# Kernel tuning notes

Hardware: AMD Instinct MI355X
Metric: run time of the kernel (lower is better)

Reference implementation:

```python
import jax, jax.numpy as jnp
import numpy as np

N_NODES = 100000
N_EDGES = 600000
D = 128          # node/edge latent dim == hs[-1]
H = 256          # hs[0] == hs[1]
LN_EPS = 1e-5


def setup_inputs() -> dict:
    key = jax.random.key(0)
    ks = jax.random.split(key, 8)
    x = jax.random.normal(ks[0], (N_NODES, D), dtype=jnp.float32)
    edge_index = jax.random.randint(ks[1], (2, N_EDGES), 0, N_NODES, dtype=jnp.int64)
    edge_attr = jax.random.normal(ks[2], (N_EDGES, D), dtype=jnp.float32)
    # MLP: Linear(256->256), SiLU, Linear(256->128); then LayerNorm(128)
    s1 = 1.0 / np.sqrt(H)
    s2 = 1.0 / np.sqrt(H)
    W1 = jax.random.uniform(ks[3], (H, H), jnp.float32, -s1, s1)
    b1 = jax.random.uniform(ks[4], (H,), jnp.float32, -s1, s1)
    W2 = jax.random.uniform(ks[5], (H, D), jnp.float32, -s2, s2)
    b2 = jax.random.uniform(ks[6], (D,), jnp.float32, -s2, s2)
    ln_gamma = jnp.ones((D,), jnp.float32)
    ln_beta = jnp.zeros((D,), jnp.float32)
    return {"x": x, "edge_index": edge_index, "edge_attr": edge_attr,
            "W1": W1, "b1": b1, "W2": W2, "b2": b2,
            "ln_gamma": ln_gamma, "ln_beta": ln_beta}


def reference(x, edge_index, edge_attr, W1, b1, W2, b2, ln_gamma, ln_beta):
    i = edge_index[0]  # destination node index (scatter target)
    # scatter-sum of edge features onto nodes: [N, D]
    agg = jax.ops.segment_sum(edge_attr, i, num_segments=x.shape[0])
    h = jnp.concatenate([x, agg], axis=-1)            # [N, 2D] == [N, H]
    h = jax.nn.silu(h @ W1 + b1)                      # Linear + SiLU
    h = h @ W2 + b2                                   # Linear (no act on last)
    # LayerNorm over last dim
    mu = jnp.mean(h, axis=-1, keepdims=True)
    var = jnp.mean(jnp.square(h - mu), axis=-1, keepdims=True)
    h = (h - mu) * jax.lax.rsqrt(var + LN_EPS) * ln_gamma + ln_beta
    return h + x                                      # residual
```

## Files before the change

kernel.cpp:

```cpp
#include <hip/hip_runtime.h>
#include <hip/hip_bf16.h>

typedef __bf16 bf16;
typedef __bf16 bf16x8 __attribute__((ext_vector_type(8)));
typedef __bf16 bf16x4v __attribute__((ext_vector_type(4)));
typedef float f32x4 __attribute__((ext_vector_type(4)));

#define NN 100000
#define NE 600000
#define SCB 2048
#define NBLK ((NN + SCB - 1) / SCB)

static __device__ __forceinline__ float silu_f(float v) {
    return v / (1.f + __expf(-v));
}

__global__ void k_probe(const void* __restrict__ gamma,
                        const void* __restrict__ eidx,
                        int* __restrict__ flags) {
    unsigned g0 = ((const unsigned*)gamma)[0];
    flags[0] = (g0 == 0x3F803F80u) ? 1 : 0;
    const int* e32 = (const int*)eidx;
    int is64 = 1;
    for (int k = 1; k < 64; k += 2)
        if (e32[k] != 0) is64 = 0;
    flags[1] = is64;
}

static __device__ __forceinline__ float load_f(const void* p, long i, int isbf) {
    return isbf ? (float)((const bf16*)p)[i] : ((const float*)p)[i];
}

static __device__ __forceinline__ bf16x8 load_row8(const void* p, long off, int isbf) {
    if (isbf) return *(const bf16x8*)((const bf16*)p + off);
    const float* f = (const float*)p + off;
    f32x4 f0 = *(const f32x4*)f;
    f32x4 f1 = *(const f32x4*)(f + 4);
    bf16x8 r;
#pragma unroll
    for (int t = 0; t < 4; t++) { r[t] = (bf16)f0[t]; r[t + 4] = (bf16)f1[t]; }
    return r;
}

__global__ __launch_bounds__(256) void k_transpose(const void* __restrict__ W1,
                                                   const void* __restrict__ W2,
                                                   bf16* __restrict__ w1t,
                                                   bf16* __restrict__ w2t,
                                                   const int* __restrict__ flags) {
    int isbf = flags[0];
    int tid = blockIdx.x * 256 + threadIdx.x;
    if (tid < 256 * 256) {
        int k = tid >> 8, n = tid & 255;
        w1t[n * 256 + k] = (bf16)load_f(W1, tid, isbf);
    } else if (tid < 256 * 256 + 256 * 128) {
        int t = tid - 256 * 256;
        int k = t >> 7, n = t & 127;
        w2t[n * 256 + k] = (bf16)load_f(W2, t, isbf);
    }
}

__global__ __launch_bounds__(256) void k_hist(const void* __restrict__ eidx,
                                              int* __restrict__ cnt,
                                              const int* __restrict__ flags) {
    int e = blockIdx.x * 256 + threadIdx.x;
    if (e >= NE) return;
    int dst = flags[1] ? (int)((const long long*)eidx)[e]
                       : ((const int*)eidx)[e];
    atomicAdd(&cnt[dst], 1);
}

__global__ __launch_bounds__(256) void k_scan1(const int* __restrict__ cnt,
                                               int* __restrict__ blksum) {
    __shared__ int red[256];
    int b = blockIdx.x, t = threadIdx.x;
    int base = b * SCB + t * 8;
    int s = 0;
#pragma unroll
    for (int i = 0; i < 8; i++) {
        int idx = base + i;
        if (idx < NN) s += cnt[idx];
    }
    red[t] = s;
    __syncthreads();
    for (int d = 128; d > 0; d >>= 1) {
        if (t < d) red[t] += red[t + d];
        __syncthreads();
    }
    if (t == 0) blksum[b] = red[0];
}

__global__ __launch_bounds__(64) void k_scan2(const int* __restrict__ blksum,
                                              int* __restrict__ blkoff) {
    int t = threadIdx.x;
    int v = (t < NBLK) ? blksum[t] : 0;
    int s = v;
#pragma unroll
    for (int d = 1; d < 64; d <<= 1) {
        int o = __shfl_up(s, d, 64);
        if (t >= d) s += o;
    }
    if (t < NBLK) blkoff[t] = s - v;
}

__global__ __launch_bounds__(256) void k_scan3(const int* __restrict__ cnt,
                                               const int* __restrict__ blkoff,
                                               int* __restrict__ off,
                                               int* __restrict__ pos) {
    __shared__ int part[256];
    int b = blockIdx.x, t = threadIdx.x;
    int base = b * SCB + t * 8;
    int v[8];
    int s = 0;
#pragma unroll
    for (int i = 0; i < 8; i++) {
        int idx = base + i;
        v[i] = (idx < NN) ? cnt[idx] : 0;
        s += v[i];
    }
    part[t] = s;
    __syncthreads();
    for (int d = 1; d < 256; d <<= 1) {
        int o = (t >= d) ? part[t - d] : 0;
        __syncthreads();
        part[t] += o;
        __syncthreads();
    }
    int run = blkoff[b] + part[t] - s;
#pragma unroll
    for (int i = 0; i < 8; i++) {
        int idx = base + i;
        if (idx < NN) { off[idx] = run; pos[idx] = run; }
        run += v[i];
    }
    if (b == 0 && t == 0) off[NN] = NE;
}

__global__ __launch_bounds__(256) void k_order(const void* __restrict__ eidx,
                                               int* __restrict__ pos,
                                               int* __restrict__ order,
                                               const int* __restrict__ flags) {
    int e = blockIdx.x * 256 + threadIdx.x;
    if (e >= NE) return;
    int dst = flags[1] ? (int)((const long long*)eidx)[e]
                       : ((const int*)eidx)[e];
    int p = atomicAdd(&pos[dst], 1);
    order[p] = e;
}

__global__ __launch_bounds__(256) void k_agg(const void* __restrict__ eattr,
                                             const int* __restrict__ order,
                                             const int* __restrict__ off,
                                             bf16* __restrict__ agg,
                                             const int* __restrict__ flags) {
    int isbf = flags[0];
    int gid = blockIdx.x * 256 + threadIdx.x;
    int node = gid >> 5;
    if (node >= NN) return;
    int c = (gid & 31) << 2;
    int beg = off[node], end = off[node + 1];
    float a0 = 0.f, a1 = 0.f, a2 = 0.f, a3 = 0.f;
    for (int e = beg; e < end; e++) {
        long id = order[e];
        if (isbf) {
            bf16x4v v = *(const bf16x4v*)((const bf16*)eattr + id * 128 + c);
            a0 += (float)v[0]; a1 += (float)v[1];
            a2 += (float)v[2]; a3 += (float)v[3];
        } else {
            f32x4 v = *(const f32x4*)((const float*)eattr + id * 128 + c);
            a0 += v[0]; a1 += v[1]; a2 += v[2]; a3 += v[3];
        }
    }
    bf16x4v r;
    r[0] = (bf16)a0; r[1] = (bf16)a1; r[2] = (bf16)a2; r[3] = (bf16)a3;
    *(bf16x4v*)(agg + (long)node * 128 + c) = r;
}

__global__ __launch_bounds__(256) void k_mlp(const void* __restrict__ x,
                                             const bf16* __restrict__ agg,
                                             const bf16* __restrict__ w1t,
                                             const void* __restrict__ b1,
                                             const bf16* __restrict__ w2t,
                                             const void* __restrict__ b2,
                                             const void* __restrict__ gamma,
                                             const void* __restrict__ beta,
                                             void* __restrict__ out,
                                             const int* __restrict__ flags) {
    __shared__ bf16 h1s[128 * 256];
    const int isbf = flags[0];
    const int tid = threadIdx.x;
    const int wave = tid >> 6, lane = tid & 63;
    const int l15 = lane & 15, quad = lane >> 4;
    const int kq = quad * 8;
    const long row0 = (long)blockIdx.x * 128;
    const int wrow = wave * 32;

    int arow[2];
#pragma unroll
    for (int i = 0; i < 2; i++) {
        long r = row0 + wrow + i * 16 + l15;
        arow[i] = (r < NN) ? (int)r : (NN - 1);
    }

    bf16x8 ax[2][4], ag[2][4];
#pragma unroll
    for (int i = 0; i < 2; i++) {
#pragma unroll
        for (int kc = 0; kc < 4; kc++) {
            ax[i][kc] = load_row8(x, (long)arow[i] * 128 + kc * 32 + kq, isbf);
            ag[i][kc] = *(const bf16x8*)(agg + (long)arow[i] * 128 + kc * 32 + kq);
        }
    }

#pragma unroll
    for (int jc = 0; jc < 4; jc++) {
        f32x4 acc[2][4] = {};
#pragma unroll
        for (int kc = 0; kc < 4; kc++) {
            bf16x8 b[4];
#pragma unroll
            for (int j = 0; j < 4; j++)
                b[j] = *(const bf16x8*)(w1t + (long)(jc * 64 + j * 16 + l15) * 256 + kc * 32 + kq);
#pragma unroll
            for (int i = 0; i < 2; i++)
#pragma unroll
                for (int j = 0; j < 4; j++)
                    acc[i][j] = __builtin_amdgcn_mfma_f32_16x16x32_bf16(ax[i][kc], b[j], acc[i][j], 0, 0, 0);
        }
#pragma unroll
        for (int kc = 0; kc < 4; kc++) {
            bf16x8 b[4];
#pragma unroll
            for (int j = 0; j < 4; j++)
                b[j] = *(const bf16x8*)(w1t + (long)(jc * 64 + j * 16 + l15) * 256 + 128 + kc * 32 + kq);
#pragma unroll
            for (int i = 0; i < 2; i++)
#pragma unroll
                for (int j = 0; j < 4; j++)
                    acc[i][j] = __builtin_amdgcn_mfma_f32_16x16x32_bf16(ag[i][kc], b[j], acc[i][j], 0, 0, 0);
        }
        float bias[4];
#pragma unroll
        for (int j = 0; j < 4; j++) bias[j] = load_f(b1, jc * 64 + j * 16 + l15, isbf);
#pragma unroll
        for (int i = 0; i < 2; i++) {
#pragma unroll
            for (int r = 0; r < 4; r++) {
                int lr = wrow + i * 16 + quad * 4 + r;
#pragma unroll
                for (int j = 0; j < 4; j++) {
                    int c = jc * 64 + j * 16 + l15;
                    int g = c >> 3, o = c & 7;
                    h1s[lr * 256 + ((g ^ (lr & 31)) << 3) + o] =
                        (bf16)silu_f(acc[i][j][r] + bias[j]);
                }
            }
        }
    }
    __syncthreads();

    f32x4 acc2[2][8] = {};
#pragma unroll
    for (int kc = 0; kc < 8; kc++) {
        bf16x8 a[2], b[8];
#pragma unroll
        for (int i = 0; i < 2; i++) {
            int lr = wrow + i * 16 + l15;
            int g = kc * 4 + quad;
            a[i] = *(const bf16x8*)(h1s + lr * 256 + ((g ^ (lr & 31)) << 3));
        }
#pragma unroll
        for (int j = 0; j < 8; j++)
            b[j] = *(const bf16x8*)(w2t + (long)(j * 16 + l15) * 256 + kc * 32 + kq);
#pragma unroll
        for (int i = 0; i < 2; i++)
#pragma unroll
            for (int j = 0; j < 8; j++)
                acc2[i][j] = __builtin_amdgcn_mfma_f32_16x16x32_bf16(a[i], b[j], acc2[i][j], 0, 0, 0);
    }

    float b2c[8], gm[8], bt[8];
#pragma unroll
    for (int j = 0; j < 8; j++) {
        int c = j * 16 + l15;
        b2c[j] = load_f(b2, c, isbf);
        gm[j] = load_f(gamma, c, isbf);
        bt[j] = load_f(beta, c, isbf);
    }

#pragma unroll
    for (int i = 0; i < 2; i++) {
#pragma unroll
        for (int r = 0; r < 4; r++) {
            long row = row0 + wrow + i * 16 + quad * 4 + r;
            float v[8], s = 0.f, s2 = 0.f;
#pragma unroll
            for (int j = 0; j < 8; j++) {
                v[j] = acc2[i][j][r] + b2c[j];
                s += v[j];
                s2 += v[j] * v[j];
            }
#pragma unroll
            for (int m = 1; m < 16; m <<= 1) {
                s += __shfl_xor(s, m, 64);
                s2 += __shfl_xor(s2, m, 64);
            }
            float mu = s * (1.f / 128.f);
            float var = s2 * (1.f / 128.f) - mu * mu;
            float rstd = rsqrtf(var + 1e-5f);
            if (row < NN) {
#pragma unroll
                for (int j = 0; j < 8; j++) {
                    int c = j * 16 + l15;
                    float o = (v[j] - mu) * rstd * gm[j] + bt[j] + load_f(x, row * 128 + c, isbf);
                    if (isbf) ((bf16*)out)[row * 128 + c] = (bf16)o;
                    else      ((float*)out)[row * 128 + c] = o;
                }
            }
        }
    }
}

extern "C" void kernel_launch(void* const* d_in, const int* in_sizes, int n_in,
                              void* d_out, int out_size, void* d_ws, size_t ws_size,
                              hipStream_t stream) {
    const void* x     = d_in[0];
    const void* eidx  = d_in[1];
    const void* eattr = d_in[2];
    const void* W1    = d_in[3];
    const void* b1    = d_in[4];
    const void* W2    = d_in[5];
    const void* b2    = d_in[6];
    const void* gamma = d_in[7];
    const void* beta  = d_in[8];

    char* ws = (char*)d_ws;
    bf16*  w1t    = (bf16*)ws;
    bf16*  w2t    = (bf16*)(ws + 131072);
    int*   flags  = (int*)(ws + 196608);
    int*   blksum = (int*)(ws + 197120);
    int*   blkoff = (int*)(ws + 197632);
    int*   cnt    = (int*)(ws + 262144);
    int*   off    = (int*)(ws + 720896);
    int*   pos    = (int*)(ws + 1179648);
    int*   order  = (int*)(ws + 1638400);
    bf16*  agg    = (bf16*)(ws + 4194304);

    k_probe<<<1, 1, 0, stream>>>(gamma, eidx, flags);
    hipMemsetAsync(cnt, 0, (size_t)NN * 4, stream);
    k_transpose<<<384, 256, 0, stream>>>(W1, W2, w1t, w2t, flags);
    k_hist<<<(NE + 255) / 256, 256, 0, stream>>>(eidx, cnt, flags);
    k_scan1<<<NBLK, 256, 0, stream>>>(cnt, blksum);
    k_scan2<<<1, 64, 0, stream>>>(blksum, blkoff);
    k_scan3<<<NBLK, 256, 0, stream>>>(cnt, blkoff, off, pos);
    k_order<<<(NE + 255) / 256, 256, 0, stream>>>(eidx, pos, order, flags);
    k_agg<<<(NN * 32) / 256, 256, 0, stream>>>(eattr, order, off, agg, flags);
    k_mlp<<<782, 256, 0, stream>>>(x, agg, w1t, b1, w2t, b2, gamma, beta, d_out, flags);
}
```

Before: 726.2 us.

## Make MLP kernel persistent with register-resident weights and LDS-staged input tiles

Rewrites the fused MLP kernel as a persistent grid of 512-thread blocks that loop over 128-row tiles. Each wave loads its slice of W1 and W2 fragments into registers once. Each tile's x and agg rows are staged cooperatively into swizzled LDS, and the output columns are split across the 8 waves, so the per-row LayerNorm sums are combined through a small LDS array. The goal is to stop re-reading weight fragments from global memory for every tile and to coalesce the input loads. In exchange it uses about 137KB of LDS per block, which likely allows only one block per CU, and adds several block-wide barriers per tile.

After: 726.9 us. About the same (+0.1%).

```diff
diff --git a/kernel.cpp b/kernel.cpp
--- a/kernel.cpp
+++ b/kernel.cpp
@@ -10,6 +10,7 @@
 #define NE 600000
 #define SCB 2048
 #define NBLK ((NN + SCB - 1) / SCB)
+#define NTILE ((NN + 127) / 128)
 
 static __device__ __forceinline__ float silu_f(float v) {
     return v / (1.f + __expf(-v));
@@ -29,17 +30,6 @@
 
 static __device__ __forceinline__ float load_f(const void* p, long i, int isbf) {
     return isbf ? (float)((const bf16*)p)[i] : ((const float*)p)[i];
-}
-
-static __device__ __forceinline__ bf16x8 load_row8(const void* p, long off, int isbf) {
-    if (isbf) return *(const bf16x8*)((const bf16*)p + off);
-    const float* f = (const float*)p + off;
-    f32x4 f0 = *(const f32x4*)f;
-    f32x4 f1 = *(const f32x4*)(f + 4);
-    bf16x8 r;
-#pragma unroll
-    for (int t = 0; t < 4; t++) { r[t] = (bf16)f0[t]; r[t + 4] = (bf16)f1[t]; }
-    return r;
 }
 
 __global__ __launch_bounds__(256) void k_transpose(const void* __restrict__ W1,
@@ -175,148 +165,166 @@
     *(bf16x4v*)(agg + (long)node * 128 + c) = r;
 }
 
-__global__ __launch_bounds__(256) void k_mlp(const void* __restrict__ x,
-                                             const bf16* __restrict__ agg,
-                                             const bf16* __restrict__ w1t,
-                                             const void* __restrict__ b1,
-                                             const bf16* __restrict__ w2t,
-                                             const void* __restrict__ b2,
-                                             const void* __restrict__ gamma,
-                                             const void* __restrict__ beta,
-                                             void* __restrict__ out,
-                                             const int* __restrict__ flags) {
+__global__ __launch_bounds__(512, 2) void k_mlp(const void* __restrict__ x,
+                                                const bf16* __restrict__ agg,
+                                                const bf16* __restrict__ w1t,
+                                                const void* __restrict__ b1,
+                                                const bf16* __restrict__ w2t,
+                                                const void* __restrict__ b2,
+                                                const void* __restrict__ gamma,
+                                                const void* __restrict__ beta,
+                                                void* __restrict__ out,
+                                                const int* __restrict__ flags) {
+    __shared__ bf16 As[128 * 256];
     __shared__ bf16 h1s[128 * 256];
+    __shared__ float2 lnred[128 * 9];
+
     const int isbf = flags[0];
     const int tid = threadIdx.x;
     const int wave = tid >> 6, lane = tid & 63;
     const int l15 = lane & 15, quad = lane >> 4;
     const int kq = quad * 8;
-    const long row0 = (long)blockIdx.x * 128;
-    const int wrow = wave * 32;
-
-    int arow[2];
-#pragma unroll
-    for (int i = 0; i < 2; i++) {
-        long r = row0 + wrow + i * 16 + l15;
-        arow[i] = (r < NN) ? (int)r : (NN - 1);
-    }
-
-    bf16x8 ax[2][4], ag[2][4];
-#pragma unroll
-    for (int i = 0; i < 2; i++) {
-#pragma unroll
-        for (int kc = 0; kc < 4; kc++) {
-            ax[i][kc] = load_row8(x, (long)arow[i] * 128 + kc * 32 + kq, isbf);
-            ag[i][kc] = *(const bf16x8*)(agg + (long)arow[i] * 128 + kc * 32 + kq);
-        }
-    }
-
-#pragma unroll
-    for (int jc = 0; jc < 4; jc++) {
-        f32x4 acc[2][4] = {};
-#pragma unroll
-        for (int kc = 0; kc < 4; kc++) {
-            bf16x8 b[4];
-#pragma unroll
-            for (int j = 0; j < 4; j++)
-                b[j] = *(const bf16x8*)(w1t + (long)(jc * 64 + j * 16 + l15) * 256 + kc * 32 + kq);
-#pragma unroll
-            for (int i = 0; i < 2; i++)
-#pragma unroll
-                for (int j = 0; j < 4; j++)
-                    acc[i][j] = __builtin_amdgcn_mfma_f32_16x16x32_bf16(ax[i][kc], b[j], acc[i][j], 0, 0, 0);
-        }
-#pragma unroll
-        for (int kc = 0; kc < 4; kc++) {
-            bf16x8 b[4];
-#pragma unroll
-            for (int j = 0; j < 4; j++)
-                b[j] = *(const bf16x8*)(w1t + (long)(jc * 64 + j * 16 + l15) * 256 + 128 + kc * 32 + kq);
-#pragma unroll
-            for (int i = 0; i < 2; i++)
-#pragma unroll
-                for (int j = 0; j < 4; j++)
-                    acc[i][j] = __builtin_amdgcn_mfma_f32_16x16x32_bf16(ag[i][kc], b[j], acc[i][j], 0, 0, 0);
-        }
-        float bias[4];
-#pragma unroll
-        for (int j = 0; j < 4; j++) bias[j] = load_f(b1, jc * 64 + j * 16 + l15, isbf);
-#pragma unroll
-        for (int i = 0; i < 2; i++) {
+
+    bf16x8 b1f[8][2], b2f[8];
+#pragma unroll
+    for (int kc = 0; kc < 8; kc++) {
+#pragma unroll
+        for (int j = 0; j < 2; j++)
+            b1f[kc][j] = *(const bf16x8*)(w1t + (long)(wave * 32 + j * 16 + l15) * 256 + kc * 32 + kq);
+        b2f[kc] = *(const bf16x8*)(w2t + (long)(wave * 16 + l15) * 256 + kc * 32 + kq);
+    }
+    float bias1[2];
+    bias1[0] = load_f(b1, wave * 32 + l15, isbf);
+    bias1[1] = load_f(b1, wave * 32 + 16 + l15, isbf);
+    const int ocol = wave * 16 + l15;
+    const float b2c = load_f(b2, ocol, isbf);
+    const float gm = load_f(gamma, ocol, isbf);
+    const float bt = load_f(beta, ocol, isbf);
+
+    for (int tile = blockIdx.x; tile < NTILE; tile += gridDim.x) {
+        const long row0 = (long)tile * 128;
+
+        if (isbf) {
+#pragma unroll
+            for (int it = 0; it < 4; it++) {
+                int idx = it * 512 + tid;
+                int r = idx >> 4, co = idx & 15;
+                long gr = row0 + r; if (gr >= NN) gr = NN - 1;
+                bf16x8 v = *(const bf16x8*)((const bf16*)x + gr * 128 + co * 8);
+                *(bf16x8*)(As + r * 256 + ((co ^ (r & 31)) << 3)) = v;
+            }
+        } else {
+#pragma unroll
+            for (int it = 0; it < 8; it++) {
+                int idx = it * 512 + tid;
+                int r = idx >> 5, cq = idx & 31;
+                long gr = row0 + r; if (gr >= NN) gr = NN - 1;
+                f32x4 v = *(const f32x4*)((const float*)x + gr * 128 + cq * 4);
+                bf16x4v h;
+#pragma unroll
+                for (int t = 0; t < 4; t++) h[t] = (bf16)v[t];
+                *(bf16x4v*)(As + r * 256 + (((cq >> 1) ^ (r & 31)) << 3) + ((cq & 1) << 2)) = h;
+            }
+        }
+#pragma unroll
+        for (int it = 0; it < 4; it++) {
+            int idx = it * 512 + tid;
+            int r = idx >> 4, co = idx & 15;
+            long gr = row0 + r; if (gr >= NN) gr = NN - 1;
+            bf16x8 v = *(const bf16x8*)(agg + gr * 128 + co * 8);
+            *(bf16x8*)(As + r * 256 + (((16 + co) ^ (r & 31)) << 3)) = v;
+        }
+        __syncthreads();
+
+#pragma unroll
+        for (int ih = 0; ih < 2; ih++) {
+            f32x4 acc[4][2] = {};
+#pragma unroll
+            for (int kc = 0; kc < 8; kc++) {
+#pragma unroll
+                for (int i2 = 0; i2 < 4; i2++) {
+                    int r = (ih * 4 + i2) * 16 + l15;
+                    bf16x8 a = *(const bf16x8*)(As + r * 256 + (((kc * 4 + quad) ^ (r & 31)) << 3));
+#pragma unroll
+                    for (int j = 0; j < 2; j++)
+                        acc[i2][j] = __builtin_amdgcn_mfma_f32_16x16x32_bf16(a, b1f[kc][j], acc[i2][j], 0, 0, 0);
+                }
+            }
+#pragma unroll
+            for (int i2 = 0; i2 < 4; i2++) {
+#pragma unroll
+                for (int j = 0; j < 2; j++) {
+#pragma unroll
+                    for (int r = 0; r < 4; r++) {
+                        int rl = (ih * 4 + i2) * 16 + quad * 4 + r;
+                        int c = wave * 32 + j * 16 + l15;
+                        h1s[rl * 256 + (((c >> 3) ^ (rl & 31)) << 3) + (c & 7)] =
+                            (bf16)silu_f(acc[i2][j][r] + bias1[j]);
+                    }
+                }
+            }
+        }
+        __syncthreads();
+
+        f32x4 acc2[8] = {};
+#pragma unroll
+        for (int kc = 0; kc < 8; kc++) {
+#pragma unroll
+            for (int i = 0; i < 8; i++) {
+                int r = i * 16 + l15;
+                bf16x8 a = *(const bf16x8*)(h1s + r * 256 + (((kc * 4 + quad) ^ (r & 31)) << 3));
+                acc2[i] = __builtin_amdgcn_mfma_f32_16x16x32_bf16(a, b2f[kc], acc2[i], 0, 0, 0);
+            }
+        }
+
+#pragma unroll
+        for (int i = 0; i < 8; i++) {
 #pragma unroll
             for (int r = 0; r < 4; r++) {
-                int lr = wrow + i * 16 + quad * 4 + r;
-#pragma unroll
-                for (int j = 0; j < 4; j++) {
-                    int c = jc * 64 + j * 16 + l15;
-                    int g = c >> 3, o = c & 7;
-                    h1s[lr * 256 + ((g ^ (lr & 31)) << 3) + o] =
-                        (bf16)silu_f(acc[i][j][r] + bias[j]);
-                }
-            }
-        }
-    }
-    __syncthreads();
-
-    f32x4 acc2[2][8] = {};
-#pragma unroll
-    for (int kc = 0; kc < 8; kc++) {
-        bf16x8 a[2], b[8];
-#pragma unroll
-        for (int i = 0; i < 2; i++) {
-            int lr = wrow + i * 16 + l15;
-            int g = kc * 4 + quad;
-            a[i] = *(const bf16x8*)(h1s + lr * 256 + ((g ^ (lr & 31)) << 3));
-        }
-#pragma unroll
-        for (int j = 0; j < 8; j++)
-            b[j] = *(const bf16x8*)(w2t + (long)(j * 16 + l15) * 256 + kc * 32 + kq);
-#pragma unroll
-        for (int i = 0; i < 2; i++)
-#pragma unroll
-            for (int j = 0; j < 8; j++)
-                acc2[i][j] = __builtin_amdgcn_mfma_f32_16x16x32_bf16(a[i], b[j], acc2[i][j], 0, 0, 0);
-    }
-
-    float b2c[8], gm[8], bt[8];
-#pragma unroll
-    for (int j = 0; j < 8; j++) {
-        int c = j * 16 + l15;
-        b2c[j] = load_f(b2, c, isbf);
-        gm[j] = load_f(gamma, c, isbf);
-        bt[j] = load_f(beta, c, isbf);
-    }
-
-#pragma unroll
-    for (int i = 0; i < 2; i++) {
-#pragma unroll
-        for (int r = 0; r < 4; r++) {
-            long row = row0 + wrow + i * 16 + quad * 4 + r;
-            float v[8], s = 0.f, s2 = 0.f;
-#pragma unroll
-            for (int j = 0; j < 8; j++) {
-                v[j] = acc2[i][j][r] + b2c[j];
-                s += v[j];
-                s2 += v[j] * v[j];
-            }
-#pragma unroll
-            for (int m = 1; m < 16; m <<= 1) {
-                s += __shfl_xor(s, m, 64);
-                s2 += __shfl_xor(s2, m, 64);
+                float v = acc2[i][r] + b2c;
+                float s = v, s2 = v * v;
+#pragma unroll
+                for (int m = 1; m < 16; m <<= 1) {
+                    s += __shfl_xor(s, m, 64);
+                    s2 += __shfl_xor(s2, m, 64);
+                }
+                if (l15 == 2 * i) {
+                    int rl = i * 16 + quad * 4 + r;
+                    lnred[rl * 9 + wave] = make_float2(s, s2);
+                }
+            }
+        }
+        __syncthreads();
+
+        if (tid < 128) {
+            float s = 0.f, s2 = 0.f;
+#pragma unroll
+            for (int w = 0; w < 8; w++) {
+                float2 p = lnred[tid * 9 + w];
+                s += p.x; s2 += p.y;
             }
             float mu = s * (1.f / 128.f);
             float var = s2 * (1.f / 128.f) - mu * mu;
-            float rstd = rsqrtf(var + 1e-5f);
-            if (row < NN) {
-#pragma unroll
-                for (int j = 0; j < 8; j++) {
-                    int c = j * 16 + l15;
-                    float o = (v[j] - mu) * rstd * gm[j] + bt[j] + load_f(x, row * 128 + c, isbf);
-                    if (isbf) ((bf16*)out)[row * 128 + c] = (bf16)o;
-                    else      ((float*)out)[row * 128 + c] = o;
-                }
-            }
-        }
+            lnred[tid * 9 + 8] = make_float2(mu, rsqrtf(var + 1e-5f));
+        }
+        __syncthreads();
+
+#pragma unroll
+        for (int i = 0; i < 8; i++) {
+#pragma unroll
+            for (int r = 0; r < 4; r++) {
+                int rl = i * 16 + quad * 4 + r;
+                long row = row0 + rl;
+                if (row < NN) {
+                    float2 mr = lnred[rl * 9 + 8];
+                    float v = acc2[i][r] + b2c;
+                    float o = (v - mr.x) * mr.y * gm + bt + load_f(x, row * 128 + ocol, isbf);
+                    if (isbf) ((bf16*)out)[row * 128 + ocol] = (bf16)o;
+                    else      ((float*)out)[row * 128 + ocol] = o;
+                }
+            }
+        }
+        __syncthreads();
     }
 }
 
@@ -354,5 +362,5 @@
     k_scan3<<<NBLK, 256, 0, stream>>>(cnt, blkoff, off, pos);
     k_order<<<(NE + 255) / 256, 256, 0, stream>>>(eidx, pos, order, flags);
     k_agg<<<(NN * 32) / 256, 256, 0, stream>>>(eattr, order, off, agg, flags);
-    k_mlp<<<782, 256, 0, stream>>>(x, agg, w1t, b1, w2t, b2, gamma, beta, d_out, flags);
-}
+    k_mlp<<<256, 512, 0, stream>>>(x, agg, w1t, b1, w2t, b2, gamma, beta, d_out, flags);
+}
```
